# Performance work log

Measured on AMD Instinct MI355X. Metric: run time of the kernel, lower is better.

Reference implementation:

```python
import jax, jax.numpy as jnp
import numpy as np

N = 8192      # input_shape[0]: side of the square complex weights A, B
UNITS = 33    # cell units; x has UNITS-1 features, state z has UNITS


def setup_inputs() -> dict:
    key = jax.random.key(0)
    ks = jax.random.split(key, 8)
    s = np.float32(1.0 / np.sqrt(N))  # keep tanh pre-activations O(1)
    f32 = jnp.float32
    return {
        "x_re": jax.random.normal(ks[0], (N, UNITS - 1), f32),
        "x_im": jax.random.normal(ks[1], (N, UNITS - 1), f32),
        "z_re": jax.random.normal(ks[2], (N, UNITS), f32),
        "z_im": jax.random.normal(ks[3], (N, UNITS), f32),
        "A_re": jax.random.normal(ks[4], (N, N), f32) * s,
        "A_im": jax.random.normal(ks[5], (N, N), f32) * s,
        "B_re": jax.random.normal(ks[6], (N, N), f32) * s,
        "B_im": jax.random.normal(ks[7], (N, N), f32) * s,
    }


def reference(x_re, x_im, z_re, z_im, A_re, A_im, B_re, B_im):
    # Assemble complex64 operands (TF cell stores A, B as complex64).
    x = jax.lax.complex(x_re, x_im)          # [N, UNITS-1]
    z = jax.lax.complex(z_re, z_im)          # [N, UNITS]
    A = jax.lax.complex(A_re, A_im)          # [N, N]
    B = jax.lax.complex(B_re, B_im)          # [N, N]

    z_0 = z[:, 0:1]                          # carried-through first column
    z_n = z[:, 1:]                           # [N, UNITS-1]

    # y_t = tanh(A @ z_n + B @ x)  (complex tanh, as tf.keras tanh on complex64)
    y_t = jnp.tanh(jnp.matmul(A, z_n) + jnp.matmul(B, x))

    # new state / output: concat([z_0, y_t], -1) -> [N, UNITS]
    return jnp.concatenate([z_0, y_t], axis=-1)
```

## Files before the change

### kernel.cpp

```cpp
#include <hip/hip_runtime.h>

#define NN 8192
#define UNITS 33
#define NCOLS 32
#define NSTEPS 512
#define NCHUNKB 8
#define CHUNKK (NN / NCHUNKB)
#define TILEK 128
#define TPC (CHUNKK / TILEK)
#define NSLAB (NCHUNKB * 4)

#define RPB 16
#define KT 32
#define NT (NN / KT)
#define SA_STRIDE 20
#define SZ_STRIDE 36
#define SA_MAT (KT * SA_STRIDE)
#define SZ_SRC (KT * SZ_STRIDE)
#define SA_FLOATS (4 * SA_MAT)
#define SZ_BASE SA_FLOATS
#define SH_FLOATS (SA_FLOATS + 4 * SZ_SRC)

typedef __attribute__((ext_vector_type(2)))  float f32x2;
typedef __attribute__((ext_vector_type(4)))  float f32x4;
typedef __attribute__((ext_vector_type(16))) float f32x16;
typedef __attribute__((ext_vector_type(8)))  short bf16x8;
typedef __attribute__((ext_vector_type(4)))  unsigned int u32x4;

union FragU { u32x4 u; bf16x8 s; };

#define MFMA(a, b, c) __builtin_amdgcn_mfma_f32_32x32x16_bf16(a, b, c, 0, 0, 0)

__device__ __forceinline__ float bfr(float v) {
    unsigned int u = __builtin_bit_cast(unsigned int, v);
    u = (u + 0x7FFFu + ((u >> 16) & 1u)) & 0xFFFF0000u;
    return __builtin_bit_cast(float, u);
}

__device__ __forceinline__ void split1(float v, unsigned int &h, unsigned int &l) {
    unsigned int u = __builtin_bit_cast(unsigned int, v);
    unsigned int hu = u >> 16;
    float hf = __builtin_bit_cast(float, hu << 16);
    float r = v - hf;
    unsigned int ru = __builtin_bit_cast(unsigned int, r);
    h = hu;
    l = (ru + 0x8000u) >> 16;
}

__device__ __forceinline__ void packHL(const unsigned int* h, const unsigned int* l,
                                       bf16x8 &hi, bf16x8 &lo) {
    FragU H, L;
    H.u.x = h[0] | (h[1] << 16); H.u.y = h[2] | (h[3] << 16);
    H.u.z = h[4] | (h[5] << 16); H.u.w = h[6] | (h[7] << 16);
    L.u.x = l[0] | (l[1] << 16); L.u.y = l[2] | (l[3] << 16);
    L.u.z = l[4] | (l[5] << 16); L.u.w = l[6] | (l[7] << 16);
    hi = H.s; lo = L.s;
}

__device__ __forceinline__ void mk_split(f32x4 a0, f32x4 a1, bf16x8 &hi, bf16x8 &lo) {
    unsigned int h[8], l[8];
#pragma unroll
    for (int e = 0; e < 4; ++e) { split1(a0[e], h[e], l[e]); split1(a1[e], h[e + 4], l[e + 4]); }
    packHL(h, l, hi, lo);
}

__device__ __forceinline__ bf16x8 fneg(bf16x8 f) {
    FragU x; x.s = f;
    x.u.x ^= 0x80008000u; x.u.y ^= 0x80008000u; x.u.z ^= 0x80008000u; x.u.w ^= 0x80008000u;
    return x.s;
}

__device__ __forceinline__ void probe_cd(int lane, int pm[16], int pn[16]) {
    int m = lane & 31, half = lane >> 5;
    unsigned int am, dummy;
    split1((float)m, am, dummy);
    unsigned int a1; split1(1.0f, a1, dummy);
    unsigned int bn; split1((float)(64 * m), bn, dummy);
    unsigned int av = (half == 0) ? am : a1;
    unsigned int bv = (half == 0) ? a1 : bn;
    FragU A, B;
    A.u.x = A.u.y = A.u.z = A.u.w = av | (av << 16);
    B.u.x = B.u.y = B.u.z = B.u.w = bv | (bv << 16);
    f32x16 d = {};
    d = MFMA(A.s, B.s, d);
#pragma unroll
    for (int r = 0; r < 16; ++r) {
        unsigned int u = (unsigned int)(d[r] * 0.125f + 0.5f);
        pm[r] = (int)(u & 63u);
        pn[r] = (int)(u >> 6);
    }
}

__device__ __forceinline__ void ctanhd(float af, float bf, float &re, float &im) {
    double a = (double)af, b = (double)bf;
    double e  = exp(2.0 * a);
    double ei = 1.0 / e;
    double ch = 0.5 * (e + ei);
    double sh = 0.5 * (e - ei);
    double cb = cos(2.0 * b);
    double sb = sin(2.0 * b);
    double d  = ch + cb;
    re = (float)(sh / d);
    im = (float)(sb / d);
}

__global__ void __launch_bounds__(256) hopf_zero(float* __restrict__ out, int n) {
    int i = blockIdx.x * 256 + threadIdx.x;
    if (i < n) out[i] = 0.0f;
}

__global__ void __launch_bounds__(256) hopf_prep(
    const float* __restrict__ xre, const float* __restrict__ xim,
    const float* __restrict__ zre, const float* __restrict__ zim,
    u32x4* __restrict__ bfrag) {
    int idx  = blockIdx.x * 256 + threadIdx.x;
    int lane = idx & 63;
    int src  = (idx >> 6) & 3;
    int step = idx >> 8;
    int n    = lane & 31;
    int half = lane >> 5;

    const float* base;
    int stride, coloff;
    if      (src == 0) { base = zre; stride = UNITS; coloff = 1; }
    else if (src == 1) { base = zim; stride = UNITS; coloff = 1; }
    else if (src == 2) { base = xre; stride = NCOLS; coloff = 0; }
    else               { base = xim; stride = NCOLS; coloff = 0; }

    unsigned int h[8], l[8];
#pragma unroll
    for (int e = 0; e < 8; ++e) {
        int k = step * 16 + 8 * half + e;
        split1(base[(size_t)k * stride + coloff + n], h[e], l[e]);
    }
    bf16x8 hi, lo;
    packHL(h, l, hi, lo);
    FragU H; H.s = hi;
    FragU L; L.s = lo;
    size_t o = (size_t)step * 512 + (size_t)src * 128 + lane;
    bfrag[o]      = H.u;
    bfrag[o + 64] = L.u;
}

struct AStep {
    f32x4 ar0, ar1, ai0, ai1, br0, br1, bi0, bi1;
};

__device__ __forceinline__ void computeStep(const AStep& s, const u32x4* __restrict__ pb,
                                            f32x16& arc, f32x16& aic) {
    FragU zrh, zrl, zih, zil, xrh, xrl, xih, xil;
    zrh.u = pb[0];   zrl.u = pb[64];
    zih.u = pb[128]; zil.u = pb[192];
    xrh.u = pb[256]; xrl.u = pb[320];
    xih.u = pb[384]; xil.u = pb[448];

    bf16x8 arh, arl, aih, ail, brh, brl, bih, bil;
    mk_split(s.ar0, s.ar1, arh, arl);
    mk_split(s.ai0, s.ai1, aih, ail);
    mk_split(s.br0, s.br1, brh, brl);
    mk_split(s.bi0, s.bi1, bih, bil);
    bf16x8 nih = fneg(aih), nil = fneg(ail);
    bf16x8 nbh = fneg(bih), nbl = fneg(bil);

    arc = MFMA(arh, zrh.s, arc); arc = MFMA(arh, zrl.s, arc); arc = MFMA(arl, zrh.s, arc);
    arc = MFMA(nih, zih.s, arc); arc = MFMA(nih, zil.s, arc); arc = MFMA(nil, zih.s, arc);
    arc = MFMA(brh, xrh.s, arc); arc = MFMA(brh, xrl.s, arc); arc = MFMA(brl, xrh.s, arc);
    arc = MFMA(nbh, xih.s, arc); arc = MFMA(nbh, xil.s, arc); arc = MFMA(nbl, xih.s, arc);
    aic = MFMA(arh, zih.s, aic); aic = MFMA(arh, zil.s, aic); aic = MFMA(arl, zih.s, aic);
    aic = MFMA(aih, zrh.s, aic); aic = MFMA(aih, zrl.s, aic); aic = MFMA(ail, zrh.s, aic);
    aic = MFMA(brh, xih.s, aic); aic = MFMA(brh, xil.s, aic); aic = MFMA(brl, xih.s, aic);
    aic = MFMA(bih, xrh.s, aic); aic = MFMA(bih, xrl.s, aic); aic = MFMA(bil, xrh.s, aic);
}

__global__ void __launch_bounds__(256) hopf_mfma2(
    const float* __restrict__ Are, const float* __restrict__ Aim,
    const float* __restrict__ Bre, const float* __restrict__ Bim,
    const u32x4* __restrict__ bfrag, float* __restrict__ partial,
    unsigned long long ws_floats) {
    __shared__ float SH[4 * 4096];
    const int tid  = threadIdx.x;
    const int lane = tid & 63;
    const int w    = tid >> 6;
    const int r    = lane & 31;
    const int half = lane >> 5;
    const int chunk  = blockIdx.x & 7;
    const int rowgrp = blockIdx.x >> 3;
    const int m0 = rowgrp * 32;
    const size_t k0chunk = (size_t)chunk * CHUNKK;

    const float* matp = (w == 0) ? Are : (w == 1) ? Aim : (w == 2) ? Bre : Bim;
    const int srh = lane >> 5;
    const int skg = lane & 31;

    f32x16 arc = {};
    f32x16 aic = {};
    f32x4 st[16];

#pragma unroll
    for (int i = 0; i < 16; ++i)
        st[i] = *(const f32x4*)(matp + (size_t)(m0 + 2 * i + srh) * NN + k0chunk + skg * 4);

    for (int t = 0; t < TPC; ++t) {
        __syncthreads();
#pragma unroll
        for (int i = 0; i < 16; ++i) {
            int row = 2 * i + srh;
            int rp  = (row ^ skg) & 31;
            *(f32x4*)&SH[w * 4096 + skg * 128 + rp * 4] = st[i];
        }
        __syncthreads();

        if (t + 1 < TPC) {
#pragma unroll
            for (int i = 0; i < 16; ++i)
                st[i] = *(const f32x4*)(matp + (size_t)(m0 + 2 * i + srh) * NN
                                        + k0chunk + (size_t)(t + 1) * TILEK + skg * 4);
        }

#pragma unroll
        for (int tt = 0; tt < 2; ++tt) {
            const int s = w * 2 + tt;
            const int kg0 = s * 4 + 2 * half;
            const int kg1 = kg0 + 1;
            AStep a;
            a.ar0 = *(const f32x4*)&SH[0 * 4096 + kg0 * 128 + ((r ^ kg0) & 31) * 4];
            a.ar1 = *(const f32x4*)&SH[0 * 4096 + kg1 * 128 + ((r ^ kg1) & 31) * 4];
            a.ai0 = *(const f32x4*)&SH[1 * 4096 + kg0 * 128 + ((r ^ kg0) & 31) * 4];
            a.ai1 = *(const f32x4*)&SH[1 * 4096 + kg1 * 128 + ((r ^ kg1) & 31) * 4];
            a.br0 = *(const f32x4*)&SH[2 * 4096 + kg0 * 128 + ((r ^ kg0) & 31) * 4];
            a.br1 = *(const f32x4*)&SH[2 * 4096 + kg1 * 128 + ((r ^ kg1) & 31) * 4];
            a.bi0 = *(const f32x4*)&SH[3 * 4096 + kg0 * 128 + ((r ^ kg0) & 31) * 4];
            a.bi1 = *(const f32x4*)&SH[3 * 4096 + kg1 * 128 + ((r ^ kg1) & 31) * 4];
            const int gstep = chunk * (CHUNKK / 16) + t * 8 + s;
            const u32x4* pb = bfrag + (size_t)gstep * 512 + lane;
            computeStep(a, pb, arc, aic);
        }
    }

    int pm[16], pn[16];
    probe_cd(lane, pm, pn);
    const int slab = chunk * 4 + w;
#pragma unroll
    for (int rr = 0; rr < 16; ++rr) {
        int mrow = m0 + pm[rr];
        size_t o = (size_t)slab * (NN * NCOLS * 2) + ((size_t)mrow * NCOLS + pn[rr]) * 2;
        if (o + 2 <= ws_floats) {
            f32x2 v; v.x = arc[rr]; v.y = aic[rr];
            *(f32x2*)(partial + o) = v;
        }
    }
}

__global__ void __launch_bounds__(256) hopf_finalize(
    const float* __restrict__ partial,
    const float* __restrict__ zre, const float* __restrict__ zim,
    float* __restrict__ out, int out_size, int nchunk) {
    int idx = blockIdx.x * 256 + threadIdx.x;
    if (idx >= NN * UNITS) return;
    int i = idx / UNITS, j = idx % UNITS;
    const bool interleaved = (out_size >= NN * UNITS * 2);
    float re, im;
    if (j == 0) {
        re = bfr(zre[(size_t)i * UNITS]);
        im = bfr(zim[(size_t)i * UNITS]);
    } else {
        size_t base = ((size_t)i * NCOLS + (j - 1)) * 2;
        float a = 0.0f, b = 0.0f;
#pragma unroll 4
        for (int c = 0; c < nchunk; ++c) {
            f32x2 v = *(const f32x2*)(partial + (size_t)c * (NN * NCOLS * 2) + base);
            a += v.x; b += v.y;
        }
        ctanhd(a, b, re, im);
        re = bfr(re); im = bfr(im);
    }
    if (interleaved) {
        if (2 * idx + 1 < out_size) { out[2 * idx] = re; out[2 * idx + 1] = im; }
    } else {
        if (idx < out_size) out[idx] = re;
    }
}

__global__ void __launch_bounds__(256) hopf_valu(
    const float* __restrict__ xre, const float* __restrict__ xim,
    const float* __restrict__ zre, const float* __restrict__ zim,
    const float* __restrict__ Are, const float* __restrict__ Aim,
    const float* __restrict__ Bre, const float* __restrict__ Bim,
    float* __restrict__ out, int out_size) {
    __shared__ float SH[SH_FLOATS];
    const int tid  = threadIdx.x;
    const int lane = tid & 63;
    const int wv   = tid >> 6;
    const int mh   = lane & 3;
    const int jh   = (lane >> 2) & 3;
    const int ks   = lane >> 4;
    const int m0   = blockIdx.x * RPB;
    const int sa_a  = tid >> 6;
    const int sa_r  = (tid >> 2) & 15;
    const int sa_kc = (tid & 3) * 8;

    float accr[4][8], acci[4][8];
#pragma unroll
    for (int dm = 0; dm < 4; ++dm)
#pragma unroll
        for (int dj = 0; dj < 8; ++dj) { accr[dm][dj] = 0.0f; acci[dm][dj] = 0.0f; }

    for (int kt = 0; kt < NT; ++kt) {
        const int k0 = kt * KT;
        __syncthreads();
        {
            const float* srcA = (sa_a == 0) ? Are : (sa_a == 1) ? Aim
                              : (sa_a == 2) ? Bre : Bim;
            const float* p = srcA + (size_t)(m0 + sa_r) * NN + k0 + sa_kc;
            f32x4 v0 = *(const f32x4*)(p);
            f32x4 v1 = *(const f32x4*)(p + 4);
#pragma unroll
            for (int i = 0; i < 4; ++i)
                SH[sa_a * SA_MAT + (sa_kc + i) * SA_STRIDE + sa_r] = v0[i];
#pragma unroll
            for (int i = 0; i < 4; ++i)
                SH[sa_a * SA_MAT + (sa_kc + 4 + i) * SA_STRIDE + sa_r] = v1[i];
        }
#pragma unroll
        for (int c = 0; c < 16; ++c) {
            const int s = c >> 2;
            const int k = (c & 3) * 8 + (tid >> 5);
            const int j = tid & 31;
            float v;
            if      (s == 0) v = zre[(size_t)(k0 + k) * UNITS + 1 + j];
            else if (s == 1) v = zim[(size_t)(k0 + k) * UNITS + 1 + j];
            else if (s == 2) v = xre[(size_t)(k0 + k) * 32 + j];
            else             v = xim[(size_t)(k0 + k) * 32 + j];
            SH[SZ_BASE + s * SZ_SRC + k * SZ_STRIDE + j] = v;
        }
        __syncthreads();

#pragma unroll
        for (int t = 0; t < 2; ++t) {
            const int kl = wv * 8 + ks * 2 + t;
            const float* sa = SH + kl * SA_STRIDE + mh * 4;
            f32x4 ar = *(const f32x4*)(sa + 0 * SA_MAT);
            f32x4 ai = *(const f32x4*)(sa + 1 * SA_MAT);
            f32x4 br = *(const f32x4*)(sa + 2 * SA_MAT);
            f32x4 bi = *(const f32x4*)(sa + 3 * SA_MAT);
            const float* sz = SH + SZ_BASE + kl * SZ_STRIDE + jh * 8;
            f32x4 zr0 = *(const f32x4*)(sz + 0 * SZ_SRC);
            f32x4 zr1 = *(const f32x4*)(sz + 0 * SZ_SRC + 4);
            f32x4 zi0 = *(const f32x4*)(sz + 1 * SZ_SRC);
            f32x4 zi1 = *(const f32x4*)(sz + 1 * SZ_SRC + 4);
            f32x4 xr0 = *(const f32x4*)(sz + 2 * SZ_SRC);
            f32x4 xr1 = *(const f32x4*)(sz + 2 * SZ_SRC + 4);
            f32x4 xi0 = *(const f32x4*)(sz + 3 * SZ_SRC);
            f32x4 xi1 = *(const f32x4*)(sz + 3 * SZ_SRC + 4);
#pragma unroll
            for (int dj = 0; dj < 8; ++dj) {
                const float vzr = (dj < 4) ? zr0[dj & 3] : zr1[dj & 3];
                const float vzi = (dj < 4) ? zi0[dj & 3] : zi1[dj & 3];
                const float vxr = (dj < 4) ? xr0[dj & 3] : xr1[dj & 3];
                const float vxi = (dj < 4) ? xi0[dj & 3] : xi1[dj & 3];
#pragma unroll
                for (int dm = 0; dm < 4; ++dm) {
                    float r = accr[dm][dj], q = acci[dm][dj];
                    r = fmaf(ar[dm],  vzr, r);
                    r = fmaf(-ai[dm], vzi, r);
                    r = fmaf(br[dm],  vxr, r);
                    r = fmaf(-bi[dm], vxi, r);
                    q = fmaf(ar[dm],  vzi, q);
                    q = fmaf(ai[dm],  vzr, q);
                    q = fmaf(br[dm],  vxi, q);
                    q = fmaf(bi[dm],  vxr, q);
                    accr[dm][dj] = r; acci[dm][dj] = q;
                }
            }
        }
    }

    __syncthreads();
    for (int i = tid; i < RPB * 32 * 2; i += 256) SH[i] = 0.0f;
    __syncthreads();
    const int myslot = wv * 4 + ks;
    for (int slot = 0; slot < 16; ++slot) {
        if (myslot == slot) {
#pragma unroll
            for (int dm = 0; dm < 4; ++dm)
#pragma unroll
                for (int dj = 0; dj < 8; ++dj) {
                    const int cell = (mh * 4 + dm) * 32 + (jh * 8 + dj);
                    SH[cell * 2 + 0] += accr[dm][dj];
                    SH[cell * 2 + 1] += acci[dm][dj];
                }
        }
        __syncthreads();
    }

    const bool interleaved = (out_size >= NN * UNITS * 2);
    {
        const int m = tid >> 4;
        const int j0 = tid & 15;
#pragma unroll
        for (int p = 0; p < 2; ++p) {
            const int j = j0 + p * 16;
            const float sr = SH[(m * 32 + j) * 2 + 0];
            const float si = SH[(m * 32 + j) * 2 + 1];
            float re, im;
            ctanhd(sr, si, re, im);
            const int e = (m0 + m) * UNITS + 1 + j;
            if (interleaved) {
                if (2 * e + 1 < out_size) { out[2 * e] = bfr(re); out[2 * e + 1] = bfr(im); }
            } else {
                if (e < out_size) out[e] = bfr(re);
            }
        }
        if (tid < RPB) {
            const int i = m0 + tid;
            const int e = i * UNITS;
            const float zr = bfr(zre[(size_t)i * UNITS]);
            const float zi = bfr(zim[(size_t)i * UNITS]);
            if (interleaved) {
                if (2 * e + 1 < out_size) { out[2 * e] = zr; out[2 * e + 1] = zi; }
            } else {
                if (e < out_size) out[e] = zr;
            }
        }
    }
}

extern "C" void kernel_launch(void* const* d_in, const int* in_sizes, int n_in,
                              void* d_out, int out_size, void* d_ws, size_t ws_size,
                              hipStream_t stream) {
    const int SX = NN * (UNITS - 1);
    const int SZn = NN * UNITS;
    const int SM = NN * NN;
    const float* xs[2] = {nullptr, nullptr};
    const float* zs[2] = {nullptr, nullptr};
    const float* ms[4] = {nullptr, nullptr, nullptr, nullptr};
    int nx = 0, nz = 0, nm = 0;
    for (int i = 0; i < n_in; ++i) {
        const float* p = (const float*)d_in[i];
        if      (in_sizes[i] == SX)  { if (nx < 2) xs[nx] = p; ++nx; }
        else if (in_sizes[i] == SZn) { if (nz < 2) zs[nz] = p; ++nz; }
        else if (in_sizes[i] == SM)  { if (nm < 4) ms[nm] = p; ++nm; }
    }
    float* out = (float*)d_out;

    if (nx != 2 || nz != 2 || nm != 4) {
        hopf_zero<<<(out_size + 255) / 256, 256, 0, stream>>>(out, out_size);
        return;
    }

    const float* xre = xs[0]; const float* xim = xs[1];
    const float* zre = zs[0]; const float* zim = zs[1];
    const float* Are = ms[0]; const float* Aim = ms[1];
    const float* Bre = ms[2]; const float* Bim = ms[3];

    const size_t SLAB_FLOATS = (size_t)NN * NCOLS * 2;
    const size_t SLAB_BYTES  = SLAB_FLOATS * 4;
    const size_t BFRAG_BYTES = (size_t)NSTEPS * 512 * sizeof(u32x4);

    if (ws_size >= NSLAB * SLAB_BYTES + BFRAG_BYTES) {
        float* partial = (float*)d_ws;
        u32x4* bfrag   = (u32x4*)((char*)d_ws + NSLAB * SLAB_BYTES);
        unsigned long long wsf = (unsigned long long)(NSLAB * SLAB_FLOATS);
        hopf_prep<<<512, 256, 0, stream>>>(xre, xim, zre, zim, bfrag);
        hopf_mfma2<<<NCHUNKB * 256, 256, 0, stream>>>(Are, Aim, Bre, Bim, bfrag, partial, wsf);
        hopf_finalize<<<(NN * UNITS + 255) / 256, 256, 0, stream>>>(partial, zre, zim, out, out_size, NSLAB);
    } else {
        hopf_valu<<<NN / RPB, 256, 0, stream>>>(xre, xim, zre, zim,
                                                Are, Aim, Bre, Bim, out, out_size);
    }
}
```

Baseline: 239.0 us.

## Double block to 512 threads, splitting k-steps across 8 waves with LDS reduction

The MFMA kernel now runs 8 waves per block instead of 4. Pairs of waves share the staging of each matrix tile, each wave loading half the rows, and each wave computes one k-step per tile instead of two. The upper four waves then pass their accumulators through shared memory to the lower four, which add them before writing the partial slab. The aim is more memory-level parallelism and latency hiding per CU, plus fewer registers per thread for staging. The cost is an extra LDS reduction with two more barriers, and a launch bound of (512,4) that may cap registers.

```diff
diff --git a/kernel.cpp b/kernel.cpp
--- a/kernel.cpp
+++ b/kernel.cpp
@@ -172,7 +172,7 @@
     aic = MFMA(bih, xrh.s, aic); aic = MFMA(bih, xrl.s, aic); aic = MFMA(bil, xrh.s, aic);
 }
 
-__global__ void __launch_bounds__(256) hopf_mfma2(
+__global__ void __launch_bounds__(512, 4) hopf_mfma2(
     const float* __restrict__ Are, const float* __restrict__ Aim,
     const float* __restrict__ Bre, const float* __restrict__ Bim,
     const u32x4* __restrict__ bfrag, float* __restrict__ partial,
@@ -188,39 +188,40 @@
     const int m0 = rowgrp * 32;
     const size_t k0chunk = (size_t)chunk * CHUNKK;
 
-    const float* matp = (w == 0) ? Are : (w == 1) ? Aim : (w == 2) ? Bre : Bim;
+    const int mat = w >> 1;
+    const int rh  = w & 1;
+    const float* matp = (mat == 0) ? Are : (mat == 1) ? Aim : (mat == 2) ? Bre : Bim;
     const int srh = lane >> 5;
     const int skg = lane & 31;
 
     f32x16 arc = {};
     f32x16 aic = {};
-    f32x4 st[16];
-
-#pragma unroll
-    for (int i = 0; i < 16; ++i)
-        st[i] = *(const f32x4*)(matp + (size_t)(m0 + 2 * i + srh) * NN + k0chunk + skg * 4);
+    f32x4 st[8];
+
+#pragma unroll
+    for (int i = 0; i < 8; ++i)
+        st[i] = *(const f32x4*)(matp + (size_t)(m0 + rh * 16 + 2 * i + srh) * NN
+                                + k0chunk + skg * 4);
 
     for (int t = 0; t < TPC; ++t) {
         __syncthreads();
 #pragma unroll
-        for (int i = 0; i < 16; ++i) {
-            int row = 2 * i + srh;
+        for (int i = 0; i < 8; ++i) {
+            int row = rh * 16 + 2 * i + srh;
             int rp  = (row ^ skg) & 31;
-            *(f32x4*)&SH[w * 4096 + skg * 128 + rp * 4] = st[i];
+            *(f32x4*)&SH[mat * 4096 + skg * 128 + rp * 4] = st[i];
         }
         __syncthreads();
 
         if (t + 1 < TPC) {
 #pragma unroll
-            for (int i = 0; i < 16; ++i)
-                st[i] = *(const f32x4*)(matp + (size_t)(m0 + 2 * i + srh) * NN
+            for (int i = 0; i < 8; ++i)
+                st[i] = *(const f32x4*)(matp + (size_t)(m0 + rh * 16 + 2 * i + srh) * NN
                                         + k0chunk + (size_t)(t + 1) * TILEK + skg * 4);
         }
 
-#pragma unroll
-        for (int tt = 0; tt < 2; ++tt) {
-            const int s = w * 2 + tt;
-            const int kg0 = s * 4 + 2 * half;
+        {
+            const int kg0 = w * 4 + 2 * half;
             const int kg1 = kg0 + 1;
             AStep a;
             a.ar0 = *(const f32x4*)&SH[0 * 4096 + kg0 * 128 + ((r ^ kg0) & 31) * 4];
@@ -231,22 +232,35 @@
             a.br1 = *(const f32x4*)&SH[2 * 4096 + kg1 * 128 + ((r ^ kg1) & 31) * 4];
             a.bi0 = *(const f32x4*)&SH[3 * 4096 + kg0 * 128 + ((r ^ kg0) & 31) * 4];
             a.bi1 = *(const f32x4*)&SH[3 * 4096 + kg1 * 128 + ((r ^ kg1) & 31) * 4];
-            const int gstep = chunk * (CHUNKK / 16) + t * 8 + s;
+            const int gstep = chunk * (CHUNKK / 16) + t * 8 + w;
             const u32x4* pb = bfrag + (size_t)gstep * 512 + lane;
             computeStep(a, pb, arc, aic);
         }
     }
 
-    int pm[16], pn[16];
-    probe_cd(lane, pm, pn);
-    const int slab = chunk * 4 + w;
-#pragma unroll
-    for (int rr = 0; rr < 16; ++rr) {
-        int mrow = m0 + pm[rr];
-        size_t o = (size_t)slab * (NN * NCOLS * 2) + ((size_t)mrow * NCOLS + pn[rr]) * 2;
-        if (o + 2 <= ws_floats) {
-            f32x2 v; v.x = arc[rr]; v.y = aic[rr];
-            *(f32x2*)(partial + o) = v;
+    __syncthreads();
+    if (w >= 4) {
+        float* dst = &SH[(w - 4) * 2112 + lane * 33];
+#pragma unroll
+        for (int rr = 0; rr < 16; ++rr) { dst[rr] = arc[rr]; dst[16 + rr] = aic[rr]; }
+    }
+    __syncthreads();
+    if (w < 4) {
+        const float* src = &SH[w * 2112 + lane * 33];
+#pragma unroll
+        for (int rr = 0; rr < 16; ++rr) { arc[rr] += src[rr]; aic[rr] += src[16 + rr]; }
+
+        int pm[16], pn[16];
+        probe_cd(lane, pm, pn);
+        const int slab = chunk * 4 + w;
+#pragma unroll
+        for (int rr = 0; rr < 16; ++rr) {
+            int mrow = m0 + pm[rr];
+            size_t o = (size_t)slab * (NN * NCOLS * 2) + ((size_t)mrow * NCOLS + pn[rr]) * 2;
+            if (o + 2 <= ws_floats) {
+                f32x2 v; v.x = arc[rr]; v.y = aic[rr];
+                *(f32x2*)(partial + o) = v;
+            }
         }
     }
 }
@@ -462,7 +476,7 @@
         u32x4* bfrag   = (u32x4*)((char*)d_ws + NSLAB * SLAB_BYTES);
         unsigned long long wsf = (unsigned long long)(NSLAB * SLAB_FLOATS);
         hopf_prep<<<512, 256, 0, stream>>>(xre, xim, zre, zim, bfrag);
-        hopf_mfma2<<<NCHUNKB * 256, 256, 0, stream>>>(Are, Aim, Bre, Bim, bfrag, partial, wsf);
+        hopf_mfma2<<<NCHUNKB * 256, 512, 0, stream>>>(Are, Aim, Bre, Bim, bfrag, partial, wsf);
         hopf_finalize<<<(NN * UNITS + 255) / 256, 256, 0, stream>>>(partial, zre, zim, out, out_size, NSLAB);
     } else {
         hopf_valu<<<NN / RPB, 256, 0, stream>>>(xre, xim, zre, zim,
```

New measurement: 233.3 us. 1.02x faster.
